# Performance work log

Measured on AMD Instinct MI355X. Metric: run time of the kernel, lower is better.

The kernel has to match this reference:

```python
import jax, jax.numpy as jnp
import numpy as np

TOPK = 180          # init kwarg topk
TOL = 3             # init kwarg tolerance_px


def setup_inputs() -> dict:
    key = jax.random.key(0)
    k1, k2, k3 = jax.random.split(key, 3)
    shape = (32, 1, 512, 512)
    return {
        "rv": jax.random.normal(k1, shape, dtype=jnp.float32),
        "ri": jax.random.normal(k2, shape, dtype=jnp.float32),
        "rf": jax.random.normal(k3, shape, dtype=jnp.float32),
    }


def reference(rv, ri, rf):
    # rf already matches rv spatially, so the interpolate branch is a no-op.
    b, c, h, w = rv.shape
    n = c * h * w
    rv_flat = rv.reshape(b, n)
    ri_flat = ri.reshape(b, n)
    rf_flat = rf.reshape(b, n)

    k = min(TOPK, n)
    _, rv_idx = jax.lax.top_k(rv_flat, k)                 # [b, k]
    _, ri_idx = jax.lax.top_k(ri_flat, k)                 # [b, k]
    _, rf_idx = jax.lax.top_k(rf_flat, min(2 * k, n))     # [b, 2k]

    rows = jnp.arange(b)[:, None]
    # union mask of VIS+IR keypoints (scatter 1.0 at top-k indices)
    src_mask = (
        jnp.zeros((b, n), jnp.float32)
        .at[rows, rv_idx].set(1.0)
        .at[rows, ri_idx].set(1.0)
    )
    src_mask = (src_mask > 0).astype(jnp.float32).reshape(b, c, h, w)

    fused_mask = (
        jnp.zeros((b, n), jnp.float32).at[rows, rf_idx].set(1.0)
    ).reshape(b, c, h, w)

    if TOL > 0:
        ksz = 2 * TOL + 1
        # max_pool2d(kernel=ksz, stride=1, padding=TOL) == dilation of the mask
        fused_mask = jax.lax.reduce_window(
            fused_mask, -jnp.inf, jax.lax.max,
            window_dimensions=(1, 1, ksz, ksz),
            window_strides=(1, 1, 1, 1),
            padding=[(0, 0), (0, 0), (TOL, TOL), (TOL, TOL)],
        )

    fused_hit = (fused_mask > 0).astype(jnp.float32)
    cover = (src_mask * fused_hit).reshape(b, -1).sum(axis=1)
    denom = jnp.maximum(src_mask.reshape(b, -1).sum(axis=1), 1.0)
    coverage = cover / denom
    return (1.0 - coverage).mean()
```

## Files before the change

kernel.cpp:

```cpp
#include <hip/hip_runtime.h>

#define N_ELEM 262144
#define SPLIT 32
#define NTS 256
#define SLICE_CAP 256
#define LSEL 2048
#define TIE_CAP 512
#define THRESH 2.5f

__device__ __forceinline__ unsigned keyOf(float f) {
    unsigned u = __float_as_uint(f);
    return (u & 0x80000000u) ? ~u : (u | 0x80000000u);
}

__device__ __forceinline__ const float* pairSrc(int p, const float* rv, const float* ri, const float* rf) {
    int t = p % 3, b = p / 3;
    return (t == 0 ? rv : (t == 1 ? ri : rf)) + (size_t)b * N_ELEM;
}

__global__ __launch_bounds__(NTS) void collect_kernel(const float* __restrict__ rv,
                                                      const float* __restrict__ ri,
                                                      const float* __restrict__ rf,
                                                      int* __restrict__ cntS,
                                                      unsigned long long* __restrict__ cand,
                                                      float* __restrict__ out,
                                                      int* __restrict__ done, int B) {
    const int p = blockIdx.x / SPLIT;
    const int s = blockIdx.x % SPLIT;
    const float4* p4 = (const float4*)pairSrc(p, rv, ri, rf) + (size_t)s * (N_ELEM / 4 / SPLIT);

    __shared__ unsigned long long buf[SLICE_CAP];
    __shared__ int s_m;
    const int tid = threadIdx.x;

    if (blockIdx.x == 0) {
        if (tid < B) done[tid] = 0;
        if (tid == B) *out = 0.0f;
    }
    if (tid == 0) s_m = 0;
    __syncthreads();

    const int base_idx = s * (N_ELEM / SPLIT);
    for (int i = tid; i < N_ELEM / 4 / SPLIT; i += NTS) {
        float4 v = p4[i];
        int pos;
        if (v.x > THRESH) { pos = atomicAdd(&s_m, 1); if (pos < SLICE_CAP) buf[pos] = ((unsigned long long)keyOf(v.x) << 32) | (unsigned)(base_idx + 4 * i + 0); }
        if (v.y > THRESH) { pos = atomicAdd(&s_m, 1); if (pos < SLICE_CAP) buf[pos] = ((unsigned long long)keyOf(v.y) << 32) | (unsigned)(base_idx + 4 * i + 1); }
        if (v.z > THRESH) { pos = atomicAdd(&s_m, 1); if (pos < SLICE_CAP) buf[pos] = ((unsigned long long)keyOf(v.z) << 32) | (unsigned)(base_idx + 4 * i + 2); }
        if (v.w > THRESH) { pos = atomicAdd(&s_m, 1); if (pos < SLICE_CAP) buf[pos] = ((unsigned long long)keyOf(v.w) << 32) | (unsigned)(base_idx + 4 * i + 3); }
    }
    __syncthreads();

    int m = s_m;
    const bool over = (m > SLICE_CAP);
    if (over) m = SLICE_CAP;
    if (tid == 0) cntS[p * SPLIT + s] = over ? -1 : m;
    unsigned long long* my = cand + (size_t)(p * SPLIT + s) * SLICE_CAP;
    for (int i = tid; i < m; i += NTS) my[i] = buf[i];
}

__global__ __launch_bounds__(NTS) void select_cov_kernel(const float* __restrict__ rv,
                                                         const float* __restrict__ ri,
                                                         const float* __restrict__ rf,
                                                         const int* __restrict__ cntS,
                                                         const unsigned long long* __restrict__ cand,
                                                         int* __restrict__ idx_out,
                                                         int* __restrict__ done,
                                                         float* __restrict__ out,
                                                         float inv_b) {
    const int p = blockIdx.x;
    const int t = p % 3;
    const int bb = p / 3;
    const int K = (t == 2) ? 360 : 180;
    int* obuf = idx_out + (size_t)p * 360;
    const int tid = threadIdx.x;

    __shared__ unsigned long long lc[LSEL];
    __shared__ unsigned hist[256];
    __shared__ int ties[TIE_CAP];
    __shared__ int soff[SPLIT]; __shared__ int scnt[SPLIT];
    __shared__ int s_total, s_bad;
    __shared__ unsigned s_p2; __shared__ int s_b2; __shared__ int s_cg2;
    __shared__ int s_on, s_tn, s_pickd; __shared__ unsigned s_pickb;
    __shared__ int s_prev;

    if (tid < 64) {
        int c = (tid < SPLIT) ? cntS[p * SPLIT + tid] : 0;
        int bad = (c < 0) ? 1 : 0;
        int cc = bad ? 0 : c;
        int v = cc;
        #pragma unroll
        for (int off = 1; off < 64; off <<= 1) {
            int u = __shfl_up(v, off, 64);
            if (tid >= off) v += u;
        }
        if (tid < SPLIT) { soff[tid] = v - cc; scnt[tid] = cc; }
        if (tid == 63) s_total = v;
        unsigned long long bm = __ballot(bad != 0);
        if (tid == 0) s_bad = (bm != 0ull) ? 1 : 0;
    }
    __syncthreads();
    const int total = s_total;
    const bool fits = (!s_bad) && (total >= K) && (total <= LSEL);

    if (fits) {
        const int sl = tid >> 3;
        const int j0 = tid & 7;
        const unsigned long long* src = cand + (size_t)(p * SPLIT + sl) * SLICE_CAP;
        const int c = scnt[sl];
        const int o = soff[sl];
        for (int j = j0; j < c; j += 8) lc[o + j] = src[j];
    }
    __syncthreads();

    const float4* p4 = (const float4*)pairSrc(p, rv, ri, rf);

    if (tid == 0) { s_p2 = 0; s_b2 = 0; s_cg2 = 0; }
    __syncthreads();

    while (s_b2 < 32) {
        hist[tid] = 0;
        __syncthreads();
        {
            const int b2 = s_b2; const unsigned p2 = s_p2;
            const int sh2 = 24 - b2;
            if (fits) {
                for (int i = tid; i < total; i += NTS) {
                    unsigned kk = (unsigned)(lc[i] >> 32);
                    bool match = (b2 == 0) || ((kk >> (32 - b2)) == p2);
                    if (match) atomicAdd(&hist[(kk >> sh2) & 255u], 1u);
                }
            } else {
                for (int i = tid; i < N_ELEM / 4; i += NTS) {
                    float4 v = p4[i];
                    unsigned kk;
                    kk = keyOf(v.x); if ((b2 == 0) || ((kk >> (32 - b2)) == p2)) atomicAdd(&hist[(kk >> sh2) & 255u], 1u);
                    kk = keyOf(v.y); if ((b2 == 0) || ((kk >> (32 - b2)) == p2)) atomicAdd(&hist[(kk >> sh2) & 255u], 1u);
                    kk = keyOf(v.z); if ((b2 == 0) || ((kk >> (32 - b2)) == p2)) atomicAdd(&hist[(kk >> sh2) & 255u], 1u);
                    kk = keyOf(v.w); if ((b2 == 0) || ((kk >> (32 - b2)) == p2)) atomicAdd(&hist[(kk >> sh2) & 255u], 1u);
                }
            }
        }
        __syncthreads();
        const unsigned r = (unsigned)(K - s_cg2);
        if (tid < 64) {
            const int l = tid;
            unsigned h0 = hist[4*l+0], h1 = hist[4*l+1], h2 = hist[4*l+2], h3 = hist[4*l+3];
            unsigned sum4 = h0 + h1 + h2 + h3;
            unsigned suf = sum4;
            #pragma unroll
            for (int off = 1; off < 64; off <<= 1) {
                unsigned u = __shfl_down(suf, off, 64);
                if (l + off < 64) suf += u;
            }
            unsigned s0 = suf, s1 = s0 - h0, s2 = s1 - h1, s3 = s2 - h2, s4 = s3 - h3;
            int d = -1; unsigned below = 0;
            if      (s3 >= r && s4 < r) { d = 4*l+3; below = s4; }
            else if (s2 >= r && s3 < r) { d = 4*l+2; below = s3; }
            else if (s1 >= r && s2 < r) { d = 4*l+1; below = s2; }
            else if (s0 >= r && s1 < r) { d = 4*l+0; below = s1; }
            if (d >= 0) { s_pickd = d; s_pickb = below; }
        }
        __syncthreads();
        if (tid == 0) {
            s_p2 = (s_p2 << 8) | (unsigned)s_pickd;
            s_cg2 += (int)s_pickb;
            s_b2 += 8;
        }
        __syncthreads();
    }

    if (tid == 0) { s_on = 0; s_tn = 0; }
    __syncthreads();

    {
        const unsigned Kth = s_p2;
        if (fits) {
            for (int i = tid; i < total; i += NTS) {
                unsigned long long e = lc[i];
                unsigned kk = (unsigned)(e >> 32);
                int idx = (int)(e & 0xffffffffu);
                if (kk > Kth) { int pos = atomicAdd(&s_on, 1); obuf[pos] = idx; }
                else if (kk == Kth) { int pos = atomicAdd(&s_tn, 1); if (pos < TIE_CAP) ties[pos] = idx; }
            }
        } else {
            for (int i = tid; i < N_ELEM / 4; i += NTS) {
                float4 v = p4[i];
                float vals[4] = {v.x, v.y, v.z, v.w};
                for (int c = 0; c < 4; ++c) {
                    unsigned kk = keyOf(vals[c]);
                    if (kk > Kth) { int pos = atomicAdd(&s_on, 1); obuf[pos] = 4 * i + c; }
                    else if (kk == Kth) { int pos = atomicAdd(&s_tn, 1); if (pos < TIE_CAP) ties[pos] = 4 * i + c; }
                }
            }
        }
    }
    __syncthreads();
    if (tid == 0) {
        int need = K - s_cg2;
        int tn = s_tn; if (tn > TIE_CAP) tn = TIE_CAP;
        int rr = need; if (rr > tn) rr = tn;
        for (int a = 0; a < rr; ++a) {
            int mb = a;
            for (int j = a + 1; j < tn; ++j) if (ties[j] < ties[mb]) mb = j;
            int tmp = ties[a]; ties[a] = ties[mb]; ties[mb] = tmp;
            obuf[s_on + a] = ties[a];
        }
        for (int a = rr; a < need; ++a) obuf[s_on + a] = (tn > 0) ? ties[0] : 0;
    }

    __threadfence();
    __syncthreads();
    if (tid == 0) s_prev = atomicAdd(&done[bb], 1);
    __syncthreads();
    if (s_prev == 2) {
        __threadfence();
        __shared__ int cnd[360]; __shared__ int fy[360]; __shared__ int fx[360];
        __shared__ int s_u, s_c;
        const int* rvI = idx_out + (size_t)(bb * 3 + 0) * 360;
        const int* riI = idx_out + (size_t)(bb * 3 + 1) * 360;
        const int* rfI = idx_out + (size_t)(bb * 3 + 2) * 360;
        for (int i = tid; i < 180; i += NTS) { cnd[i] = rvI[i]; cnd[180 + i] = riI[i]; }
        for (int i = tid; i < 360; i += NTS) { int v = rfI[i]; fy[i] = v >> 9; fx[i] = v & 511; }
        if (tid == 0) { s_u = 0; s_c = 0; }
        __syncthreads();

        int myu = 0, myc = 0;
        for (int i = tid; i < 360; i += NTS) {
            const int v = cnd[i];
            const int y = v >> 9, x = v & 511;
            int dup = 0;
            #pragma unroll 8
            for (int j = 0; j < 360; ++j) dup |= (int)((j < i) & (cnd[j] == v));
            int cov = 0;
            #pragma unroll 8
            for (int j = 0; j < 360; ++j) {
                int dy = y - fy[j]; dy = (dy < 0) ? -dy : dy;
                int dx = x - fx[j]; dx = (dx < 0) ? -dx : dx;
                cov |= (int)((dy <= 3) & (dx <= 3));
            }
            if (!dup) { myu += 1; myc += cov; }
        }
        if (myu) atomicAdd(&s_u, myu);
        if (myc) atomicAdd(&s_c, myc);
        __syncthreads();
        if (tid == 0) {
            float denom = (float)(s_u > 0 ? s_u : 1);
            float loss = 1.0f - (float)s_c / denom;
            atomicAdd(out, loss * inv_b);
        }
    }
}

extern "C" void kernel_launch(void* const* d_in, const int* in_sizes, int n_in,
                              void* d_out, int out_size, void* d_ws, size_t ws_size,
                              hipStream_t stream) {
    const float* rv = (const float*)d_in[0];
    const float* ri = (const float*)d_in[1];
    const float* rf = (const float*)d_in[2];
    float* out = (float*)d_out;

    const int B = in_sizes[0] / N_ELEM;
    const int P = 3 * B;

    char* ws = (char*)d_ws;
    int* cntS = (int*)ws;
    int* done = (int*)(ws + (size_t)P * SPLIT * 4);
    int* idx_buf = (int*)(ws + (size_t)P * SPLIT * 4 + (size_t)B * 4);
    size_t fixed = (size_t)P * SPLIT * 4 + (size_t)B * 4 + (size_t)P * 360 * 4;
    fixed = (fixed + 7) & ~(size_t)7;
    unsigned long long* cand = (unsigned long long*)(ws + fixed);

    collect_kernel<<<P * SPLIT, NTS, 0, stream>>>(rv, ri, rf, cntS, cand, out, done, B);
    select_cov_kernel<<<P, NTS, 0, stream>>>(rv, ri, rf, cntS, cand, idx_buf, done, out, 1.0f / (float)B);
}
```

Before: 170.3 us.

## Use shared-memory bitmaps for coverage and split candidate keys/indices

The final per-batch coverage step swaps the O(360x360) pairwise dedup and distance checks for bitmaps in shared memory. The fused top-k set goes into a 512x512 bitmap, and source points are deduplicated with atomicOr on a half-image bitmap. Coverage is then found by testing 7 rows of masked words. Candidate entries are also stored as separate key and index arrays, which cuts LDS traffic in the histogram passes. The cost is a large 48KB shared buffer that may reduce occupancy, plus extra clearing work for the bitmaps.

Result: faster. 143.8 us (-15.6%).

```diff
diff --git a/kernel.cpp b/kernel.cpp
--- a/kernel.cpp
+++ b/kernel.cpp
@@ -75,14 +75,16 @@
     int* obuf = idx_out + (size_t)p * 360;
     const int tid = threadIdx.x;
 
-    __shared__ unsigned long long lc[LSEL];
+    __shared__ __align__(16) unsigned char smem[49152];
+    unsigned* lcKey = (unsigned*)smem;
+    unsigned* lcIdx = (unsigned*)(smem + 8192);
     __shared__ unsigned hist[256];
     __shared__ int ties[TIE_CAP];
     __shared__ int soff[SPLIT]; __shared__ int scnt[SPLIT];
     __shared__ int s_total, s_bad;
     __shared__ unsigned s_p2; __shared__ int s_b2; __shared__ int s_cg2;
     __shared__ int s_on, s_tn, s_pickd; __shared__ unsigned s_pickb;
-    __shared__ int s_prev;
+    __shared__ int s_prev, s_u, s_c;
 
     if (tid < 64) {
         int c = (tid < SPLIT) ? cntS[p * SPLIT + tid] : 0;
@@ -109,7 +111,11 @@
         const unsigned long long* src = cand + (size_t)(p * SPLIT + sl) * SLICE_CAP;
         const int c = scnt[sl];
         const int o = soff[sl];
-        for (int j = j0; j < c; j += 8) lc[o + j] = src[j];
+        for (int j = j0; j < c; j += 8) {
+            unsigned long long e = src[j];
+            lcKey[o + j] = (unsigned)(e >> 32);
+            lcIdx[o + j] = (unsigned)(e & 0xffffffffu);
+        }
     }
     __syncthreads();
 
@@ -126,7 +132,7 @@
             const int sh2 = 24 - b2;
             if (fits) {
                 for (int i = tid; i < total; i += NTS) {
-                    unsigned kk = (unsigned)(lc[i] >> 32);
+                    unsigned kk = lcKey[i];
                     bool match = (b2 == 0) || ((kk >> (32 - b2)) == p2);
                     if (match) atomicAdd(&hist[(kk >> sh2) & 255u], 1u);
                 }
@@ -177,9 +183,8 @@
         const unsigned Kth = s_p2;
         if (fits) {
             for (int i = tid; i < total; i += NTS) {
-                unsigned long long e = lc[i];
-                unsigned kk = (unsigned)(e >> 32);
-                int idx = (int)(e & 0xffffffffu);
+                unsigned kk = lcKey[i];
+                int idx = (int)lcIdx[i];
                 if (kk > Kth) { int pos = atomicAdd(&s_on, 1); obuf[pos] = idx; }
                 else if (kk == Kth) { int pos = atomicAdd(&s_tn, 1); if (pos < TIE_CAP) ties[pos] = idx; }
             }
@@ -215,31 +220,54 @@
     __syncthreads();
     if (s_prev == 2) {
         __threadfence();
-        __shared__ int cnd[360]; __shared__ int fy[360]; __shared__ int fx[360];
-        __shared__ int s_u, s_c;
+        unsigned* rfbm  = (unsigned*)smem;
+        unsigned* srcbm = (unsigned*)(smem + 32768);
         const int* rvI = idx_out + (size_t)(bb * 3 + 0) * 360;
         const int* riI = idx_out + (size_t)(bb * 3 + 1) * 360;
         const int* rfI = idx_out + (size_t)(bb * 3 + 2) * 360;
-        for (int i = tid; i < 180; i += NTS) { cnd[i] = rvI[i]; cnd[180 + i] = riI[i]; }
-        for (int i = tid; i < 360; i += NTS) { int v = rfI[i]; fy[i] = v >> 9; fx[i] = v & 511; }
+
+        for (int i = tid; i < 8192; i += NTS) rfbm[i] = 0;
         if (tid == 0) { s_u = 0; s_c = 0; }
         __syncthreads();
+        for (int i = tid; i < 360; i += NTS) {
+            int v = rfI[i];
+            atomicOr(&rfbm[v >> 5], 1u << (v & 31));
+        }
+        __syncthreads();
 
         int myu = 0, myc = 0;
-        for (int i = tid; i < 360; i += NTS) {
-            const int v = cnd[i];
-            const int y = v >> 9, x = v & 511;
-            int dup = 0;
-            #pragma unroll 8
-            for (int j = 0; j < 360; ++j) dup |= (int)((j < i) & (cnd[j] == v));
-            int cov = 0;
-            #pragma unroll 8
-            for (int j = 0; j < 360; ++j) {
-                int dy = y - fy[j]; dy = (dy < 0) ? -dy : dy;
-                int dx = x - fx[j]; dx = (dx < 0) ? -dx : dx;
-                cov |= (int)((dy <= 3) & (dx <= 3));
-            }
-            if (!dup) { myu += 1; myc += cov; }
+        for (int h = 0; h < 2; ++h) {
+            for (int i = tid; i < 4096; i += NTS) srcbm[i] = 0;
+            __syncthreads();
+            for (int i = tid; i < 360; i += NTS) {
+                int v = (i < 180) ? rvI[i] : riI[i - 180];
+                int y = v >> 9, x = v & 511;
+                if ((y >> 8) == h) {
+                    unsigned bit = 1u << (v & 31);
+                    unsigned old = atomicOr(&srcbm[(v >> 5) & 4095], bit);
+                    if (!(old & bit)) {
+                        myu++;
+                        int lo = x - 3; if (lo < 0) lo = 0;
+                        int hi = x + 3; if (hi > 511) hi = 511;
+                        int k0 = lo >> 5, k1 = hi >> 5;
+                        unsigned m0, m1;
+                        if (k0 == k1) { m0 = ((1u << (hi - lo + 1)) - 1u) << (lo & 31); m1 = 0u; }
+                        else          { m0 = 0xffffffffu << (lo & 31); m1 = (1u << ((hi & 31) + 1)) - 1u; }
+                        unsigned cov = 0;
+                        #pragma unroll
+                        for (int dy = -3; dy <= 3; ++dy) {
+                            int yy = y + dy;
+                            if (yy >= 0 && yy < 512) {
+                                const unsigned* row = &rfbm[yy << 4];
+                                cov |= (row[k0] & m0);
+                                if (k1 != k0) cov |= (row[k1] & m1);
+                            }
+                        }
+                        myc += (cov != 0u) ? 1 : 0;
+                    }
+                }
+            }
+            __syncthreads();
         }
         if (myu) atomicAdd(&s_u, myu);
         if (myc) atomicAdd(&s_c, myc);
```
